# Performance work log

Hardware: AMD Instinct MI355X
Metric: run time of the kernel (lower is better)

Reference implementation:

```python
import jax, jax.numpy as jnp
import numpy as np

B, S, E = 32, 577, 1024
H = 16
D = E // H  # head_size = 64


def setup_inputs() -> dict:
    key = jax.random.key(0)
    ks = jax.random.split(key, 5)
    scale_init = E ** -0.5
    x = jax.random.normal(ks[0], (B, S, E), dtype=jnp.float32)
    # Per-head projection weights. torch Linear weight is [out,in]; we store
    # [H, E, D] so that x @ Wq[h] == torch_linear(x) with weight Wq[h].T.
    Wq = jax.random.normal(ks[1], (H, E, D), dtype=jnp.float32) * scale_init
    Wk = jax.random.normal(ks[2], (H, E, D), dtype=jnp.float32) * scale_init
    Wv = jax.random.normal(ks[3], (H, E, D), dtype=jnp.float32) * scale_init
    # Output projection (with bias, as in nn.Linear default)
    Wo = jax.random.normal(ks[4], (E, E), dtype=jnp.float32) * scale_init
    bo = jnp.zeros((E,), dtype=jnp.float32)
    return {"x": x, "Wq": Wq, "Wk": Wk, "Wv": Wv, "Wo": Wo, "bo": bo}


def reference(x, Wq, Wk, Wv, Wo, bo):
    scale = D ** -0.5
    # Per-head QKV projections, vectorized over heads: [B,H,S,D]
    q = jnp.einsum('bse,hed->bhsd', x, Wq)
    k = jnp.einsum('bse,hed->bhsd', x, Wk)
    v = jnp.einsum('bse,hed->bhsd', x, Wv)
    scores = jnp.einsum('bhsd,bhtd->bhst', q, k) * scale  # [B,H,S,S]
    attn = jax.nn.softmax(scores, axis=-1)
    out = jnp.einsum('bhst,bhtd->bhsd', attn, v)  # [B,H,S,D]
    # Concat heads: head h occupies slice [h*D:(h+1)*D], matching torch.cat order
    out = out.transpose(0, 2, 1, 3).reshape(B, S, E)
    return out @ Wo.T + bo  # torch Linear: x @ W.T + b
```

## Files before the change

### kernel.cpp

```cpp
#include <hip/hip_runtime.h>
#include <hip/hip_bf16.h>
#include <stdint.h>

using sh8    = __attribute__((ext_vector_type(8))) short;
using f32x4  = __attribute__((ext_vector_type(4))) float;
using f32x16 = __attribute__((ext_vector_type(16))) float;

#define MFMA16(a, b, c) __builtin_amdgcn_mfma_f32_16x16x32_bf16(a, b, c, 0, 0, 0)
#define EXP2F(x) __builtin_amdgcn_exp2f(x)

static constexpr int BB = 32, SS = 577, HH = 16;
static constexpr int MM = BB * SS;
static constexpr int SPAD = 640;
static constexpr float QSCALE = 0.18033688011112042f;

__device__ __forceinline__ ushort f2b(float f) {
  union { float f; uint32_t u; } v{f};
  uint32_t r = v.u + 0x7FFFu + ((v.u >> 16) & 1u);
  return (ushort)(r >> 16);
}

#if __has_builtin(__builtin_amdgcn_cvt_pk_bf16_f32)
typedef __attribute__((ext_vector_type(2))) __bf16 bf16x2_t;
__device__ __forceinline__ uint32_t pk_bf16(float a, float b) {
  union { bf16x2_t v; uint32_t u; } c;
  c.v = __builtin_amdgcn_cvt_pk_bf16_f32(a, b);
  return c.u;
}
#else
__device__ __forceinline__ uint32_t pk_bf16(float a, float b) {
  return (uint32_t)f2b(a) | ((uint32_t)f2b(b) << 16);
}
#endif

__device__ __forceinline__ void gld16(const ushort* g, ushort* l) {
  __builtin_amdgcn_global_load_lds(
      (const __attribute__((address_space(1))) uint32_t*)g,
      (__attribute__((address_space(3))) uint32_t*)l, 16, 0, 0);
}

__global__ __launch_bounds__(256)
void convert2_f32_bf16(const float* __restrict__ a, ushort* __restrict__ oa, int na4,
                       const float* __restrict__ b, ushort* __restrict__ ob, int nb4) {
  const int total = na4 + nb4;
  const int stride = gridDim.x * 256;
  for (int i = blockIdx.x * 256 + threadIdx.x; i < total; i += stride) {
    const float4 f = (i < na4) ? ((const float4*)a)[i] : ((const float4*)b)[i - na4];
    ushort4 u;
    u.x = f2b(f.x); u.y = f2b(f.y); u.z = f2b(f.z); u.w = f2b(f.w);
    if (i < na4) ((ushort4*)oa)[i] = u;
    else         ((ushort4*)ob)[i - na4] = u;
  }
}

__global__ __launch_bounds__(256)
void convert_wqkv(const float* __restrict__ Wq, const float* __restrict__ Wk,
                  const float* __restrict__ Wv, ushort* __restrict__ Wt) {
  __shared__ ushort T[64 * 72];
  const int tid = threadIdx.x;
  const int kt = blockIdx.x, sh = blockIdx.y;
  const int sel = sh >> 4, h = sh & 15;
  const float* W = (sel == 0) ? Wq : ((sel == 1) ? Wk : Wv);
  const float qs = (sel == 0) ? QSCALE : 1.0f;
  const int rr = tid >> 4;
  const int rc = (tid & 15) * 4;
#pragma unroll
  for (int p = 0; p < 64; p += 16) {
    const float4 f = *(const float4*)(W + (size_t)h * 65536 + (size_t)(kt * 64 + p + rr) * 64 + rc);
    ushort4 u;
    u.x = f2b(f.x * qs); u.y = f2b(f.y * qs); u.z = f2b(f.z * qs); u.w = f2b(f.w * qs);
    *(ushort4*)&T[(p + rr) * 72 + rc] = u;
  }
  __syncthreads();
  const int dd = tid >> 2;
  const int c16 = (tid & 3) * 16;
  sh8 v0, v1;
#pragma unroll
  for (int j = 0; j < 8; j++) v0[j] = (short)T[(c16 + j) * 72 + dd];
#pragma unroll
  for (int j = 0; j < 8; j++) v1[j] = (short)T[(c16 + 8 + j) * 72 + dd];
  ushort* op = Wt + ((size_t)sel * 1024 + h * 64 + dd) * 1024 + kt * 64 + c16;
  *(sh8*)op = v0;
  *(sh8*)(op + 8) = v1;
}

template <int MODE>
__global__ __launch_bounds__(256)
void gemm_bt(const ushort* __restrict__ A, const ushort* __restrict__ Bt,
             ushort* __restrict__ Cb, float* __restrict__ Cf,
             const float* __restrict__ bias, int M, int N, int K) {
  __shared__ ushort Al[128 * 64];
  __shared__ ushort Bl[128 * 64];
  const int tid = threadIdx.x;
  const int lane = tid & 63, w = tid >> 6;
  const int l15 = lane & 15, quad = lane >> 4;
  const int wm = (w >> 1) * 64, wn = (w & 1) * 64;

  const int nwg = gridDim.x * gridDim.y;
  const int orig = blockIdx.y * gridDim.x + blockIdx.x;
  const int wgid = (orig & 7) * (nwg >> 3) + (orig >> 3);
  const int m0 = (wgid / gridDim.x) * 128;
  const int n0 = (wgid % gridDim.x) * 128;

  f32x4 acc[4][4];
#pragma unroll
  for (int i = 0; i < 4; i++)
#pragma unroll
    for (int j = 0; j < 4; j++) acc[i][j] = f32x4{0.f, 0.f, 0.f, 0.f};

  const int rbase = tid >> 3;
  const int swzc = ((tid & 7) ^ (rbase & 7)) * 8;
  const ushort* Ag[4]; const ushort* Bg[4];
  ushort* lA[4]; ushort* lB[4];
#pragma unroll
  for (int i = 0; i < 4; i++) {
    Ag[i] = A + (size_t)min(m0 + i * 32 + rbase, M - 1) * K + swzc;
    Bg[i] = Bt + (size_t)(n0 + i * 32 + rbase) * K + swzc;
    lA[i] = &Al[(i * 256 + tid) * 8];
    lB[i] = &Bl[(i * 256 + tid) * 8];
  }
  const int swz = l15 & 7;
  const int c0 = (quad ^ swz) * 8;
  const int c1 = ((quad + 4) ^ swz) * 8;
  const int arow = (wm + l15) * 64;
  const int brow = (wn + l15) * 64;

  for (int k0 = 0; k0 < K; k0 += 64) {
    __syncthreads();
#pragma unroll
    for (int i = 0; i < 4; i++) {
      gld16(Ag[i] + k0, lA[i]);
      gld16(Bg[i] + k0, lB[i]);
    }
    __syncthreads();
#pragma unroll
    for (int kc = 0; kc < 2; kc++) {
      const int ck = (kc == 0) ? c0 : c1;
      sh8 af[4], bfr[4];
#pragma unroll
      for (int i = 0; i < 4; i++) af[i] = *(const sh8*)&Al[arow + i * 1024 + ck];
#pragma unroll
      for (int j = 0; j < 4; j++) bfr[j] = *(const sh8*)&Bl[brow + j * 1024 + ck];
#pragma unroll
      for (int i = 0; i < 4; i++)
#pragma unroll
        for (int j = 0; j < 4; j++) acc[i][j] = MFMA16(bfr[j], af[i], acc[i][j]);
    }
  }

#pragma unroll
  for (int i = 0; i < 4; i++) {
    const int row = m0 + wm + i * 16 + l15;
    const bool ok = row < M;
#pragma unroll
    for (int j = 0; j < 4; j++) {
      const int col0 = n0 + wn + j * 16 + quad * 4;
      if (MODE == 0) {
        uint2 pk;
        pk.x = pk_bf16(acc[i][j][0], acc[i][j][1]);
        pk.y = pk_bf16(acc[i][j][2], acc[i][j][3]);
        if (ok) *(uint2*)&Cb[(size_t)row * N + col0] = pk;
      } else {
        const float4 b4 = *(const float4*)&bias[col0];
        float4 v;
        v.x = acc[i][j][0] + b4.x; v.y = acc[i][j][1] + b4.y;
        v.z = acc[i][j][2] + b4.z; v.w = acc[i][j][3] + b4.w;
        if (ok) *(float4*)&Cf[(size_t)row * N + col0] = v;
      }
    }
  }
}

__global__ __launch_bounds__(256)
void transpose_v(const ushort* __restrict__ QKV, ushort* __restrict__ Vtg) {
  __shared__ ushort T[64 * 72];
  const int tid = threadIdx.x;
  const int st = blockIdx.x, bh = blockIdx.y;
  const int b = bh >> 4, h = bh & 15;
  const int sr = tid >> 3;
  const int sc = (tid & 7) * 8;
#pragma unroll
  for (int p = 0; p < 64; p += 32) {
    const int s = st * 64 + p + sr;
    uint4 d = uint4{0u, 0u, 0u, 0u};
    if (s < SS) d = *(const uint4*)(QKV + ((size_t)b * SS + s) * 3072 + 2048 + h * 64 + sc);
    *(uint4*)&T[(p + sr) * 72 + sc] = d;
  }
  __syncthreads();
  const int dd = tid >> 2;
  const int s16 = (tid & 3) * 16;
  sh8 v0, v1;
#pragma unroll
  for (int j = 0; j < 8; j++) v0[j] = (short)T[(s16 + j) * 72 + dd];
#pragma unroll
  for (int j = 0; j < 8; j++) v1[j] = (short)T[(s16 + 8 + j) * 72 + dd];
  ushort* outp = Vtg + ((size_t)bh * 64 + dd) * SPAD + st * 64 + s16;
  *(sh8*)outp = v0;
  *(sh8*)(outp + 8) = v1;
}

__global__ __launch_bounds__(256)
void flash_attn(const ushort* __restrict__ QKV, const ushort* __restrict__ Vtg,
                ushort* __restrict__ Ob) {
  __shared__ ushort Kl[2][64 * 64];
  __shared__ ushort Vl[2][64 * 64];
  __shared__ ushort Pl[128 * 72];
  const int tid = threadIdx.x;
  const int lane = tid & 63, w = tid >> 6;
  const int l15 = lane & 15, quad = lane >> 4;
  const int qb = blockIdx.x, bh = blockIdx.y;
  const int b = bh >> 4, h = bh & 15;

  sh8 qf[2][2];
#pragma unroll
  for (int g = 0; g < 2; g++) {
    const int qr = qb * 128 + w * 32 + g * 16 + l15;
    const ushort* qrow = QKV + ((size_t)b * SS + min(qr, SS - 1)) * 3072 + h * 64;
    qf[g][0] = *(const sh8*)(qrow + quad * 8);
    qf[g][1] = *(const sh8*)(qrow + 32 + quad * 8);
  }

  sh8 ones;
#pragma unroll
  for (int j = 0; j < 8; j++) ones[j] = (short)0x3F80;

  f32x4 o[2][4];
  f32x4 acc_l[2];
#pragma unroll
  for (int g = 0; g < 2; g++) {
    acc_l[g] = f32x4{0.f, 0.f, 0.f, 0.f};
#pragma unroll
    for (int t = 0; t < 4; t++) o[g][t] = f32x4{0.f, 0.f, 0.f, 0.f};
  }

  const int r0 = tid >> 3;
  const int swzs = ((tid & 7) ^ (r0 & 7)) * 8;
  const ushort* Kg = QKV + (size_t)b * SS * 3072 + 1024 + h * 64 + swzs;
  const ushort* Vg0 = Vtg + ((size_t)bh * 64 + r0) * SPAD + swzs;
  const ushort* Vg1 = Vtg + ((size_t)bh * 64 + 32 + r0) * SPAD + swzs;
  ushort* lK0[2] = { &Kl[0][tid * 8],         &Kl[1][tid * 8] };
  ushort* lK1[2] = { &Kl[0][(256 + tid) * 8], &Kl[1][(256 + tid) * 8] };
  ushort* lV0[2] = { &Vl[0][tid * 8],         &Vl[1][tid * 8] };
  ushort* lV1[2] = { &Vl[0][(256 + tid) * 8], &Vl[1][(256 + tid) * 8] };

  const int swz = l15 & 7;
  const int ca0 = (quad ^ swz) * 8;
  const int ca1 = ((quad + 4) ^ swz) * 8;
  ushort* plw[2] = { &Pl[(w * 32 + l15) * 72], &Pl[(w * 32 + 16 + l15) * 72] };

  gld16(Kg + (size_t)min(r0, SS - 1) * 3072, lK0[0]);
  gld16(Kg + (size_t)min(32 + r0, SS - 1) * 3072, lK1[0]);
  gld16(Vg0, lV0[0]);
  gld16(Vg1, lV1[0]);
  __syncthreads();

  for (int kt = 0; kt < 10; kt++) {
    const int cur = kt & 1;
    if (kt < 9) {
      const int kb1 = (kt + 1) * 64;
      gld16(Kg + (size_t)min(kb1 + r0, SS - 1) * 3072, lK0[cur ^ 1]);
      gld16(Kg + (size_t)min(kb1 + 32 + r0, SS - 1) * 3072, lK1[cur ^ 1]);
      gld16(Vg0 + kb1, lV0[cur ^ 1]);
      gld16(Vg1 + kb1, lV1[cur ^ 1]);
    }
    const ushort* Kc = &Kl[cur][0];
    const ushort* Vc = &Vl[cur][0];

#pragma unroll
    for (int tn = 0; tn < 4; tn++) {
      const int kr = tn * 16 + l15;
      const sh8 k0 = *(const sh8*)&Kc[kr * 64 + ca0];
      const sh8 k1 = *(const sh8*)&Kc[kr * 64 + ca1];
#pragma unroll
      for (int g = 0; g < 2; g++) {
        f32x4 s = f32x4{0.f, 0.f, 0.f, 0.f};
        s = MFMA16(k0, qf[g][0], s);
        s = MFMA16(k1, qf[g][1], s);
        if (kt == 9) {
#pragma unroll
          for (int r = 0; r < 4; r++)
            if ((tn * 16 + quad * 4 + r) != 0) s[r] = -1e30f;
        }
        uint2 pp;
        pp.x = pk_bf16(EXP2F(s[0]), EXP2F(s[1]));
        pp.y = pk_bf16(EXP2F(s[2]), EXP2F(s[3]));
        *(uint2*)(plw[g] + tn * 16 + quad * 4) = pp;
      }
    }
    sh8 pa[2][2];
#pragma unroll
    for (int g = 0; g < 2; g++) {
      pa[g][0] = *(const sh8*)(plw[g] + quad * 8);
      pa[g][1] = *(const sh8*)(plw[g] + 32 + quad * 8);
      acc_l[g] = MFMA16(ones, pa[g][0], acc_l[g]);
      acc_l[g] = MFMA16(ones, pa[g][1], acc_l[g]);
    }
#pragma unroll
    for (int t = 0; t < 4; t++) {
      const int vr = t * 16 + l15;
      const sh8 v0 = *(const sh8*)&Vc[vr * 64 + ca0];
      const sh8 v1 = *(const sh8*)&Vc[vr * 64 + ca1];
#pragma unroll
      for (int g = 0; g < 2; g++) {
        o[g][t] = MFMA16(v0, pa[g][0], o[g][t]);
        o[g][t] = MFMA16(v1, pa[g][1], o[g][t]);
      }
    }

    if (kt < 9) __syncthreads();
  }

#pragma unroll
  for (int g = 0; g < 2; g++) {
    const float inv = 1.0f / acc_l[g][0];
    const int s = qb * 128 + w * 32 + g * 16 + l15;
    if (s < SS) {
      ushort* op = Ob + ((size_t)b * SS + s) * 1024 + h * 64 + quad * 4;
#pragma unroll
      for (int t = 0; t < 4; t++) {
        uint2 ov;
        ov.x = pk_bf16(o[g][t][0] * inv, o[g][t][1] * inv);
        ov.y = pk_bf16(o[g][t][2] * inv, o[g][t][3] * inv);
        *(uint2*)(op + t * 16) = ov;
      }
    }
  }
}

extern "C" void kernel_launch(void* const* d_in, const int* in_sizes, int n_in,
                              void* d_out, int out_size, void* d_ws, size_t ws_size,
                              hipStream_t stream) {
  const float* x  = (const float*)d_in[0];
  const float* Wq = (const float*)d_in[1];
  const float* Wk = (const float*)d_in[2];
  const float* Wv = (const float*)d_in[3];
  const float* Wo = (const float*)d_in[4];
  const float* bo = (const float*)d_in[5];
  float* out = (float*)d_out;

  ushort* Xb  = (ushort*)d_ws;
  ushort* Wt  = Xb  + (size_t)MM * 1024;
  ushort* Wob = Wt  + (size_t)3072 * 1024;
  ushort* QKV = Wob + (size_t)1024 * 1024;
  ushort* Vtg = QKV + (size_t)MM * 3072;
  ushort* Ob  = Xb;

  convert2_f32_bf16<<<4096, 256, 0, stream>>>(x, Xb, MM * 1024 / 4, Wo, Wob, 1024 * 1024 / 4);
  convert_wqkv<<<dim3(16, 48), 256, 0, stream>>>(Wq, Wk, Wv, Wt);
  gemm_bt<0><<<dim3(24, 145), 256, 0, stream>>>(Xb, Wt, QKV, nullptr, nullptr, MM, 3072, 1024);
  transpose_v<<<dim3(10, 512), 256, 0, stream>>>(QKV, Vtg);
  flash_attn<<<dim3(5, 512), 256, 0, stream>>>(QKV, Vtg, Ob);
  gemm_bt<1><<<dim3(8, 145), 256, 0, stream>>>(Ob, Wob, nullptr, out, bo, MM, 1024, 1024);
}
```

Baseline: 439.8 us.

## Peel the last key row out of flash attention and add MFMA priority hints

The flash attention loop now runs over 9 key tiles of 64 instead of 10. The single leftover key (row 576) is handled after the loop with a scalar dot product, shuffle reductions, and a rank-1 update of the output and the normaliser, which removes a nearly empty tenth tile and its masking. s_setprio raises wave priority around the MFMA blocks to improve interleaving with other waves. Separately, the GEMM drops its XCD-aware block remapping for plain row-major indexing, which may hurt L2 locality.

```diff
diff --git a/kernel.cpp b/kernel.cpp
--- a/kernel.cpp
+++ b/kernel.cpp
@@ -8,6 +8,8 @@
 
 #define MFMA16(a, b, c) __builtin_amdgcn_mfma_f32_16x16x32_bf16(a, b, c, 0, 0, 0)
 #define EXP2F(x) __builtin_amdgcn_exp2f(x)
+#define PRIO1() __builtin_amdgcn_s_setprio(1)
+#define PRIO0() __builtin_amdgcn_s_setprio(0)
 
 static constexpr int BB = 32, SS = 577, HH = 16;
 static constexpr int MM = BB * SS;
@@ -18,6 +20,11 @@
   union { float f; uint32_t u; } v{f};
   uint32_t r = v.u + 0x7FFFu + ((v.u >> 16) & 1u);
   return (ushort)(r >> 16);
+}
+
+__device__ __forceinline__ float bf2f(ushort u) {
+  union { uint32_t u; float f; } v{(uint32_t)u << 16};
+  return v.f;
 }
 
 #if __has_builtin(__builtin_amdgcn_cvt_pk_bf16_f32)
@@ -95,12 +102,7 @@
   const int lane = tid & 63, w = tid >> 6;
   const int l15 = lane & 15, quad = lane >> 4;
   const int wm = (w >> 1) * 64, wn = (w & 1) * 64;
-
-  const int nwg = gridDim.x * gridDim.y;
-  const int orig = blockIdx.y * gridDim.x + blockIdx.x;
-  const int wgid = (orig & 7) * (nwg >> 3) + (orig >> 3);
-  const int m0 = (wgid / gridDim.x) * 128;
-  const int n0 = (wgid % gridDim.x) * 128;
+  const int m0 = blockIdx.y * 128, n0 = blockIdx.x * 128;
 
   f32x4 acc[4][4];
 #pragma unroll
@@ -205,6 +207,7 @@
   __shared__ ushort Kl[2][64 * 64];
   __shared__ ushort Vl[2][64 * 64];
   __shared__ ushort Pl[128 * 72];
+  __shared__ ushort vt576[64];
   const int tid = threadIdx.x;
   const int lane = tid & 63, w = tid >> 6;
   const int l15 = lane & 15, quad = lane >> 4;
@@ -248,18 +251,19 @@
   const int ca1 = ((quad + 4) ^ swz) * 8;
   ushort* plw[2] = { &Pl[(w * 32 + l15) * 72], &Pl[(w * 32 + 16 + l15) * 72] };
 
-  gld16(Kg + (size_t)min(r0, SS - 1) * 3072, lK0[0]);
-  gld16(Kg + (size_t)min(32 + r0, SS - 1) * 3072, lK1[0]);
+  gld16(Kg + (size_t)r0 * 3072, lK0[0]);
+  gld16(Kg + (size_t)(32 + r0) * 3072, lK1[0]);
   gld16(Vg0, lV0[0]);
   gld16(Vg1, lV1[0]);
+  if (tid < 64) vt576[tid] = QKV[((size_t)b * SS + 576) * 3072 + 2048 + h * 64 + tid];
   __syncthreads();
 
-  for (int kt = 0; kt < 10; kt++) {
+  for (int kt = 0; kt < 9; kt++) {
     const int cur = kt & 1;
-    if (kt < 9) {
+    if (kt < 8) {
       const int kb1 = (kt + 1) * 64;
-      gld16(Kg + (size_t)min(kb1 + r0, SS - 1) * 3072, lK0[cur ^ 1]);
-      gld16(Kg + (size_t)min(kb1 + 32 + r0, SS - 1) * 3072, lK1[cur ^ 1]);
+      gld16(Kg + (size_t)(kb1 + r0) * 3072, lK0[cur ^ 1]);
+      gld16(Kg + (size_t)(kb1 + 32 + r0) * 3072, lK1[cur ^ 1]);
       gld16(Vg0 + kb1, lV0[cur ^ 1]);
       gld16(Vg1 + kb1, lV1[cur ^ 1]);
     }
@@ -271,19 +275,20 @@
       const int kr = tn * 16 + l15;
       const sh8 k0 = *(const sh8*)&Kc[kr * 64 + ca0];
       const sh8 k1 = *(const sh8*)&Kc[kr * 64 + ca1];
+      f32x4 sv[2];
+      PRIO1();
 #pragma unroll
       for (int g = 0; g < 2; g++) {
-        f32x4 s = f32x4{0.f, 0.f, 0.f, 0.f};
-        s = MFMA16(k0, qf[g][0], s);
-        s = MFMA16(k1, qf[g][1], s);
-        if (kt == 9) {
-#pragma unroll
-          for (int r = 0; r < 4; r++)
-            if ((tn * 16 + quad * 4 + r) != 0) s[r] = -1e30f;
-        }
+        sv[g] = f32x4{0.f, 0.f, 0.f, 0.f};
+        sv[g] = MFMA16(k0, qf[g][0], sv[g]);
+        sv[g] = MFMA16(k1, qf[g][1], sv[g]);
+      }
+      PRIO0();
+#pragma unroll
+      for (int g = 0; g < 2; g++) {
         uint2 pp;
-        pp.x = pk_bf16(EXP2F(s[0]), EXP2F(s[1]));
-        pp.y = pk_bf16(EXP2F(s[2]), EXP2F(s[3]));
+        pp.x = pk_bf16(EXP2F(sv[g][0]), EXP2F(sv[g][1]));
+        pp.y = pk_bf16(EXP2F(sv[g][2]), EXP2F(sv[g][3]));
         *(uint2*)(plw[g] + tn * 16 + quad * 4) = pp;
       }
     }
@@ -292,6 +297,10 @@
     for (int g = 0; g < 2; g++) {
       pa[g][0] = *(const sh8*)(plw[g] + quad * 8);
       pa[g][1] = *(const sh8*)(plw[g] + 32 + quad * 8);
+    }
+    PRIO1();
+#pragma unroll
+    for (int g = 0; g < 2; g++) {
       acc_l[g] = MFMA16(ones, pa[g][0], acc_l[g]);
       acc_l[g] = MFMA16(ones, pa[g][1], acc_l[g]);
     }
@@ -306,13 +315,38 @@
         o[g][t] = MFMA16(v1, pa[g][1], o[g][t]);
       }
     }
-
-    if (kt < 9) __syncthreads();
-  }
-
+    PRIO0();
+
+    if (kt < 8) __syncthreads();
+  }
+
+  const ushort* k576p = QKV + ((size_t)b * SS + 576) * 3072 + 1024 + h * 64;
+  const sh8 kta = *(const sh8*)(k576p + quad * 8);
+  const sh8 ktb = *(const sh8*)(k576p + 32 + quad * 8);
+  float p5[2];
 #pragma unroll
   for (int g = 0; g < 2; g++) {
-    const float inv = 1.0f / acc_l[g][0];
+    float s = 0.f;
+#pragma unroll
+    for (int j = 0; j < 8; j++) {
+      s += bf2f((ushort)qf[g][0][j]) * bf2f((ushort)kta[j]);
+      s += bf2f((ushort)qf[g][1][j]) * bf2f((ushort)ktb[j]);
+    }
+    s += __shfl_xor(s, 16);
+    s += __shfl_xor(s, 32);
+    p5[g] = EXP2F(s);
+  }
+#pragma unroll
+  for (int g = 0; g < 2; g++)
+#pragma unroll
+    for (int t = 0; t < 4; t++)
+#pragma unroll
+      for (int r = 0; r < 4; r++)
+        o[g][t][r] += p5[g] * bf2f(vt576[t * 16 + quad * 4 + r]);
+
+#pragma unroll
+  for (int g = 0; g < 2; g++) {
+    const float inv = 1.0f / (acc_l[g][0] + p5[g]);
     const int s = qb * 128 + w * 32 + g * 16 + l15;
     if (s < SS) {
       ushort* op = Ob + ((size_t)b * SS + s) * 1024 + h * 64 + quad * 4;
```

After: 426.1 us. 1.03x faster.
